# Performance work log

Measured on AMD Instinct MI355X. Metric: run time of the kernel, lower is better.

Reference implementation:

```python
import jax, jax.numpy as jnp
import numpy as np

B, S, H, D, M = 8, 1024, 16, 64, 1024


def setup_inputs() -> dict:
    key = jax.random.key(0)
    ks = jax.random.split(key, 7)
    return {
        "query_tensor": jax.random.normal(ks[0], (B, S, H, D), dtype=jnp.float32),
        "key_tensor": jax.random.normal(ks[1], (B, S, H, D), dtype=jnp.float32),
        "value_tensor": jax.random.normal(ks[2], (B, H, S, D), dtype=jnp.float32),
        "qm_b": jax.random.randint(ks[3], (M,), 0, B, dtype=jnp.int32),
        "qm_s": jax.random.randint(ks[4], (M,), 0, S, dtype=jnp.int32),
        "km_b": jax.random.randint(ks[5], (M,), 0, B, dtype=jnp.int32),
        "km_s": jax.random.randint(ks[6], (M,), 0, S, dtype=jnp.int32),
    }


def reference(query_tensor, key_tensor, value_tensor, qm_b, qm_s, km_b, km_s):
    b, s, h, d = query_tensor.shape
    scale = 1.0 / jnp.sqrt(jnp.asarray(d, jnp.float32))
    # (B,H,Sq,Sk) = Q K^T / sqrt(d); q,k given as (B,S,H,D)
    corr = jnp.einsum('bqhd,bkhd->bhqk', query_tensor, key_tensor) * scale
    # masks: query_mask zeros whole rows, key_mask zeros whole columns
    row_masked = jnp.zeros((b, s), dtype=bool).at[qm_b, qm_s].set(True)
    col_masked = jnp.zeros((b, s), dtype=bool).at[km_b, km_s].set(True)
    masked = row_masked[:, None, :, None] | col_masked[:, None, None, :]
    corr = jnp.where(masked, jnp.asarray(-1e10, corr.dtype), corr)
    attn = jax.nn.softmax(corr, axis=-1)
    # value_tensor is already (B,H,S,D) per the original (no permute applied)
    return jnp.einsum('bhqk,bhkd->bhqd', attn, value_tensor)
```

## Files before the change

### kernel.cpp

```cpp
#include <hip/hip_runtime.h>
#include <stdint.h>

#define GLOBAL_AS __attribute__((address_space(1)))
#define LDS_AS __attribute__((address_space(3)))

namespace {
constexpr int Bn = 8, Sn = 1024, Hn = 16, Dn = 64, Mn = 1024;
constexpr int BQ = 128;
constexpr int TK = 64;
constexpr int NT = Sn / TK;
constexpr int LDE = 72;
constexpr int TILE_SH = 2 * 64 * LDE;
constexpr size_t BLOB_BYTES = (size_t)Bn * Hn * NT * TILE_SH * 2;
constexpr size_t ROWM_OFF = BLOB_BYTES;
constexpr float kSC = 0.125f * 1.4426950408889634f;

using f32x16 = __attribute__((ext_vector_type(16))) float;
using s16x4 = __attribute__((ext_vector_type(4))) short;
using s16x8 = __attribute__((ext_vector_type(8))) short;

__device__ inline unsigned pk2(float a, float b) {
    union { __bf16 h[2]; unsigned u; } x;
    x.h[0] = (__bf16)a; x.h[1] = (__bf16)b;
    return x.u;
}

#if __has_builtin(__builtin_amdgcn_exp2f)
#define EXP2F __builtin_amdgcn_exp2f
#else
#define EXP2F exp2f
#endif
}

__global__ __launch_bounds__(256) void convert3(
    const float* __restrict__ K, const float* __restrict__ V,
    unsigned short* __restrict__ blob,
    const int* __restrict__ qmb, const int* __restrict__ qms,
    const int* __restrict__ kmb, const int* __restrict__ kms,
    unsigned int* __restrict__ wsm)
{
    __shared__ float Vl[64 * 65];
    const int t = threadIdx.x;
    const int kt = blockIdx.x, h = blockIdx.y, b = blockIdx.z;

    if (kt == 0 && h == 0 && b == 0) {
        #pragma unroll
        for (int i = 0; i < 9; ++i) wsm[t + 256 * i] = 0;
        __syncthreads();
        unsigned char* rowm = (unsigned char*)wsm;
        unsigned long long* colbits = (unsigned long long*)(wsm + 2048);
        #pragma unroll
        for (int i = 0; i < 4; ++i) {
            const int idx = t + 256 * i;
            rowm[qmb[idx] * Sn + qms[idx]] = 1;
            atomicOr(&colbits[kmb[idx] * NT + (kms[idx] >> 6)], 1ull << (kms[idx] & 63));
        }
    }

    unsigned short* out = blob + ((size_t)((b * Hn + h) * NT + kt)) * TILE_SH;
    const int key = t >> 2, dg = (t & 3) * 16;
    {
        const float* kp = K + (((size_t)b * Sn + kt * TK + key) * Hn + h) * Dn + dg;
        uint2 w[4];
        #pragma unroll
        for (int j = 0; j < 4; ++j) {
            float4 v = *(const float4*)(kp + j * 4);
            w[j].x = pk2(v.x, v.y); w[j].y = pk2(v.z, v.w);
        }
        uint2* o = (uint2*)&out[key * LDE + dg];
        #pragma unroll
        for (int j = 0; j < 4; ++j) o[j] = w[j];
    }
    {
        const float* vp = V + (((size_t)b * Hn + h) * Sn + kt * TK + key) * Dn + dg;
        #pragma unroll
        for (int j = 0; j < 4; ++j) {
            float4 v = *(const float4*)(vp + j * 4);
            Vl[(dg + j * 4 + 0) * 65 + key] = v.x;
            Vl[(dg + j * 4 + 1) * 65 + key] = v.y;
            Vl[(dg + j * 4 + 2) * 65 + key] = v.z;
            Vl[(dg + j * 4 + 3) * 65 + key] = v.w;
        }
    }
    __syncthreads();
    {
        const int d = t >> 2, kc = (t & 3) * 16;
        float tmp[16];
        #pragma unroll
        for (int i = 0; i < 16; ++i) tmp[i] = Vl[d * 65 + kc + i];
        uint2* o = (uint2*)&out[64 * LDE + d * LDE + kc];
        #pragma unroll
        for (int j = 0; j < 4; ++j) {
            uint2 w; w.x = pk2(tmp[j * 4 + 0], tmp[j * 4 + 1]);
            w.y = pk2(tmp[j * 4 + 2], tmp[j * 4 + 3]);
            o[j] = w;
        }
    }
}

__global__ __launch_bounds__(256, 4) void attn4(
    const float* __restrict__ Q, const unsigned short* __restrict__ blob,
    const unsigned char* __restrict__ rowm,
    const unsigned long long* __restrict__ colbits,
    float* __restrict__ Out)
{
    __shared__ unsigned short KV[TILE_SH];
    const int t = threadIdx.x;
    const int wave = t >> 6, lane = t & 63;
    const int l31 = lane & 31, q2 = lane >> 5;
    const int bh = blockIdx.x, b = bh >> 4, h = bh & 15;
    const int qb = blockIdx.y * BQ + wave * 32;

    s16x8 qf[4];
    {
        const float* qp = Q + (((size_t)b * Sn + qb + l31) * Hn + h) * Dn + q2 * 8;
        #pragma unroll
        for (int st = 0; st < 4; ++st) {
            float4 a = *(const float4*)(qp + st * 16);
            float4 c = *(const float4*)(qp + st * 16 + 4);
            union { unsigned w[4]; s16x8 v; } f;
            f.w[0] = pk2(a.x * kSC, a.y * kSC);
            f.w[1] = pk2(a.z * kSC, a.w * kSC);
            f.w[2] = pk2(c.x * kSC, c.y * kSC);
            f.w[3] = pk2(c.z * kSC, c.w * kSC);
            qf[st] = f.v;
        }
    }
    const bool rmb = rowm[b * Sn + qb + l31] != 0;
    const float rmONE = rmb ? 1.0f : 0.0f;
    const unsigned rmKEEP = rmb ? 0u : 0xFFFFFFFFu;

    f32x16 O[2];
    #pragma unroll
    for (int dt = 0; dt < 2; ++dt)
        #pragma unroll
        for (int i = 0; i < 16; ++i) O[dt][i] = 0.0f;
    float lsum = 0.0f;

    const unsigned short* tile0 = blob + (size_t)bh * NT * TILE_SH;

    for (int kt = 0; kt < NT; ++kt) {
        __syncthreads();
        {
            const GLOBAL_AS unsigned int* g =
                (const GLOBAL_AS unsigned int*)(tile0 + (size_t)kt * TILE_SH);
            LDS_AS unsigned int* l = (LDS_AS unsigned int*)KV;
            #pragma unroll
            for (int j = 0; j < 4; ++j)
                __builtin_amdgcn_global_load_lds(g + j * 1024 + t * 4,
                                                 l + j * 1024 + t * 4, 16, 0, 0);
            if (t < 128)
                __builtin_amdgcn_global_load_lds(g + 4096 + t * 4,
                                                 l + 4096 + t * 4, 16, 0, 0);
        }
        const unsigned long long cmask = colbits[b * NT + kt];
        __syncthreads();

        #pragma unroll
        for (int ct = 0; ct < 2; ++ct) {
            s16x8 kf[4];
            #pragma unroll
            for (int st = 0; st < 4; ++st)
                kf[st] = *(const s16x8*)&KV[(ct * 32 + l31) * LDE + st * 16 + q2 * 8];
            const unsigned ncm = ~(((unsigned)(cmask >> (ct * 32))) >> (q2 * 4));

            f32x16 sc;
            #pragma unroll
            for (int i = 0; i < 16; ++i) sc[i] = 0.0f;
            #pragma unroll
            for (int st = 0; st < 4; ++st)
                sc = __builtin_amdgcn_mfma_f32_32x32x16_bf16(kf[st], qf[st], sc, 0, 0, 0);

            const unsigned keep = ncm & rmKEEP;
            unsigned u[8];
            #pragma unroll
            for (int c = 0; c < 4; ++c) {
                float p[4];
                #pragma unroll
                for (int j = 0; j < 4; ++j) {
                    float e = EXP2F(sc[4 * c + j]);
                    unsigned m = (unsigned)__builtin_amdgcn_sbfe((int)keep, 8 * c + j, 1);
                    p[j] = __uint_as_float(__float_as_uint(e) & m) + rmONE;
                }
                lsum += (p[0] + p[1]) + (p[2] + p[3]);
                u[2 * c]     = pk2(p[0], p[1]);
                u[2 * c + 1] = pk2(p[2], p[3]);
            }
            s16x8 P[2];
            union { unsigned w[4]; s16x8 v; } f0, f1;
            f0.w[0] = u[0]; f0.w[1] = u[1]; f0.w[2] = u[2]; f0.w[3] = u[3];
            f1.w[0] = u[4]; f1.w[1] = u[5]; f1.w[2] = u[6]; f1.w[3] = u[7];
            P[0] = f0.v;
            P[1] = f1.v;

            const unsigned short* Vt = &KV[64 * LDE];
            #pragma unroll
            for (int dt = 0; dt < 2; ++dt)
                #pragma unroll
                for (int ch = 0; ch < 2; ++ch) {
                    const int base = (dt * 32 + l31) * LDE + ct * 32 + ch * 16 + q2 * 4;
                    s16x4 lo = *(const s16x4*)&Vt[base];
                    s16x4 hi = *(const s16x4*)&Vt[base + 8];
                    s16x8 vf = __builtin_shufflevector(lo, hi, 0, 1, 2, 3, 4, 5, 6, 7);
                    O[dt] = __builtin_amdgcn_mfma_f32_32x32x16_bf16(P[ch], vf, O[dt], 0, 0, 0);
                }
        }
    }

    const float invs = 1.0f / (lsum + __shfl_xor(lsum, 32, 64));
    float* op = Out + ((size_t)(b * Hn + h)) * Sn * Dn;
    #pragma unroll
    for (int reg = 0; reg < 16; ++reg) {
        const int qrow = (reg & 3) + 8 * (reg >> 2) + 4 * q2;
        const float invl = __shfl(invs, qrow, 64);
        const int q = qb + qrow;
        #pragma unroll
        for (int dt = 0; dt < 2; ++dt)
            op[(size_t)q * Dn + dt * 32 + l31] = O[dt][reg] * invl;
    }
}

extern "C" void kernel_launch(void* const* d_in, const int* in_sizes, int n_in,
                              void* d_out, int out_size, void* d_ws, size_t ws_size,
                              hipStream_t stream) {
    (void)in_sizes; (void)n_in; (void)out_size; (void)ws_size;
    const float* Q = (const float*)d_in[0];
    const float* K = (const float*)d_in[1];
    const float* V = (const float*)d_in[2];
    const int* qmb = (const int*)d_in[3];
    const int* qms = (const int*)d_in[4];
    const int* kmb = (const int*)d_in[5];
    const int* kms = (const int*)d_in[6];
    float* Out = (float*)d_out;

    unsigned short* blob = (unsigned short*)d_ws;
    unsigned int* wsm = (unsigned int*)(void*)((char*)d_ws + ROWM_OFF);
    const unsigned char* rowm = (const unsigned char*)wsm;
    const unsigned long long* colbits = (const unsigned long long*)(wsm + 2048);

    convert3<<<dim3(NT, Hn, Bn), 256, 0, stream>>>(K, V, blob, qmb, qms, kmb, kms, wsm);
    attn4<<<dim3(Bn * Hn, Sn / BQ), 256, 0, stream>>>(Q, blob, rowm, colbits, Out);
}
```

Measured before the change: 194.3 us.

## Fold key/query masks into an extra MFMA step via a bias column

Column-mask bits are written as a -1e8 bf16 bias into the padding columns of each K tile, and the query row mask is applied by zeroing the Q scale and adding a fifth Q fragment (1 or 0). Together these let a fifth MFMA step apply both masks inside the score computation, so the per-element bit-extract masking in the softmax loop goes away. The V transpose is permuted so each lane can fetch its fragment with one 16-byte LDS load instead of two 8-byte loads. Mask construction moves to a separate single-block kernel ahead of the convert kernel, which adds a launch and a serial dependency in exchange for 25% more QK MFMA work.

Result: faster. 186.1 us (-4.2%).

```diff
diff --git a/kernel.cpp b/kernel.cpp
--- a/kernel.cpp
+++ b/kernel.cpp
@@ -14,9 +14,9 @@
 constexpr size_t BLOB_BYTES = (size_t)Bn * Hn * NT * TILE_SH * 2;
 constexpr size_t ROWM_OFF = BLOB_BYTES;
 constexpr float kSC = 0.125f * 1.4426950408889634f;
+constexpr float kBIAS = -1e8f;
 
 using f32x16 = __attribute__((ext_vector_type(16))) float;
-using s16x4 = __attribute__((ext_vector_type(4))) short;
 using s16x8 = __attribute__((ext_vector_type(8))) short;
 
 __device__ inline unsigned pk2(float a, float b) {
@@ -32,32 +32,32 @@
 #endif
 }
 
-__global__ __launch_bounds__(256) void convert3(
-    const float* __restrict__ K, const float* __restrict__ V,
-    unsigned short* __restrict__ blob,
+__global__ __launch_bounds__(1024) void masks_k(
     const int* __restrict__ qmb, const int* __restrict__ qms,
     const int* __restrict__ kmb, const int* __restrict__ kms,
     unsigned int* __restrict__ wsm)
 {
+    const int t = threadIdx.x;
+    wsm[t] = 0; wsm[t + 1024] = 0;
+    if (t < 256) wsm[t + 2048] = 0;
+    __syncthreads();
+    unsigned char* rowm = (unsigned char*)wsm;
+    unsigned long long* colbits = (unsigned long long*)(wsm + 2048);
+    rowm[qmb[t] * Sn + qms[t]] = 1;
+    atomicOr(&colbits[kmb[t] * NT + (kms[t] >> 6)], 1ull << (kms[t] & 63));
+}
+
+__global__ __launch_bounds__(256) void convert4(
+    const float* __restrict__ K, const float* __restrict__ V,
+    unsigned short* __restrict__ blob,
+    const unsigned long long* __restrict__ colbits)
+{
     __shared__ float Vl[64 * 65];
     const int t = threadIdx.x;
     const int kt = blockIdx.x, h = blockIdx.y, b = blockIdx.z;
-
-    if (kt == 0 && h == 0 && b == 0) {
-        #pragma unroll
-        for (int i = 0; i < 9; ++i) wsm[t + 256 * i] = 0;
-        __syncthreads();
-        unsigned char* rowm = (unsigned char*)wsm;
-        unsigned long long* colbits = (unsigned long long*)(wsm + 2048);
-        #pragma unroll
-        for (int i = 0; i < 4; ++i) {
-            const int idx = t + 256 * i;
-            rowm[qmb[idx] * Sn + qms[idx]] = 1;
-            atomicOr(&colbits[kmb[idx] * NT + (kms[idx] >> 6)], 1ull << (kms[idx] & 63));
-        }
-    }
-
     unsigned short* out = blob + ((size_t)((b * Hn + h) * NT + kt)) * TILE_SH;
+    const unsigned long long cb = colbits[b * NT + kt];
+
     const int key = t >> 2, dg = (t & 3) * 16;
     {
         const float* kp = K + (((size_t)b * Sn + kt * TK + key) * Hn + h) * Dn + dg;
@@ -70,6 +70,12 @@
         uint2* o = (uint2*)&out[key * LDE + dg];
         #pragma unroll
         for (int j = 0; j < 4; ++j) o[j] = w[j];
+    }
+    if ((t & 3) == 3) {
+        const float bias = ((cb >> key) & 1ull) ? kBIAS : 0.0f;
+        uint2 w; w.x = pk2(bias, 0.0f); w.y = 0u;
+        *(uint2*)&out[key * LDE + 64] = w;
+        *(uint2*)&out[key * LDE + 68] = (uint2){0u, 0u};
     }
     {
         const float* vp = V + (((size_t)b * Hn + h) * Sn + kt * TK + key) * Dn + dg;
@@ -88,20 +94,21 @@
         float tmp[16];
         #pragma unroll
         for (int i = 0; i < 16; ++i) tmp[i] = Vl[d * 65 + kc + i];
+        const int perm[16] = {0, 1, 2, 3, 8, 9, 10, 11, 4, 5, 6, 7, 12, 13, 14, 15};
         uint2* o = (uint2*)&out[64 * LDE + d * LDE + kc];
         #pragma unroll
         for (int j = 0; j < 4; ++j) {
-            uint2 w; w.x = pk2(tmp[j * 4 + 0], tmp[j * 4 + 1]);
-            w.y = pk2(tmp[j * 4 + 2], tmp[j * 4 + 3]);
+            uint2 w;
+            w.x = pk2(tmp[perm[4 * j + 0]], tmp[perm[4 * j + 1]]);
+            w.y = pk2(tmp[perm[4 * j + 2]], tmp[perm[4 * j + 3]]);
             o[j] = w;
         }
     }
 }
 
-__global__ __launch_bounds__(256, 4) void attn4(
+__global__ __launch_bounds__(256, 4) void attn5(
     const float* __restrict__ Q, const unsigned short* __restrict__ blob,
     const unsigned char* __restrict__ rowm,
-    const unsigned long long* __restrict__ colbits,
     float* __restrict__ Out)
 {
     __shared__ unsigned short KV[TILE_SH];
@@ -111,7 +118,10 @@
     const int bh = blockIdx.x, b = bh >> 4, h = bh & 15;
     const int qb = blockIdx.y * BQ + wave * 32;
 
-    s16x8 qf[4];
+    const bool rmb = rowm[b * Sn + qb + l31] != 0;
+    const float qscale = rmb ? 0.0f : kSC;
+
+    s16x8 qf[5];
     {
         const float* qp = Q + (((size_t)b * Sn + qb + l31) * Hn + h) * Dn + q2 * 8;
         #pragma unroll
@@ -119,16 +129,17 @@
             float4 a = *(const float4*)(qp + st * 16);
             float4 c = *(const float4*)(qp + st * 16 + 4);
             union { unsigned w[4]; s16x8 v; } f;
-            f.w[0] = pk2(a.x * kSC, a.y * kSC);
-            f.w[1] = pk2(a.z * kSC, a.w * kSC);
-            f.w[2] = pk2(c.x * kSC, c.y * kSC);
-            f.w[3] = pk2(c.z * kSC, c.w * kSC);
+            f.w[0] = pk2(a.x * qscale, a.y * qscale);
+            f.w[1] = pk2(a.z * qscale, a.w * qscale);
+            f.w[2] = pk2(c.x * qscale, c.y * qscale);
+            f.w[3] = pk2(c.z * qscale, c.w * qscale);
             qf[st] = f.v;
         }
-    }
-    const bool rmb = rowm[b * Sn + qb + l31] != 0;
-    const float rmONE = rmb ? 1.0f : 0.0f;
-    const unsigned rmKEEP = rmb ? 0u : 0xFFFFFFFFu;
+        union { unsigned w[4]; s16x8 v; } f5;
+        f5.w[0] = (q2 == 0) ? pk2(rmb ? 0.0f : 1.0f, 0.0f) : 0u;
+        f5.w[1] = 0u; f5.w[2] = 0u; f5.w[3] = 0u;
+        qf[4] = f5.v;
+    }
 
     f32x16 O[2];
     #pragma unroll
@@ -153,38 +164,32 @@
                 __builtin_amdgcn_global_load_lds(g + 4096 + t * 4,
                                                  l + 4096 + t * 4, 16, 0, 0);
         }
-        const unsigned long long cmask = colbits[b * NT + kt];
         __syncthreads();
 
         #pragma unroll
         for (int ct = 0; ct < 2; ++ct) {
-            s16x8 kf[4];
-            #pragma unroll
-            for (int st = 0; st < 4; ++st)
+            s16x8 kf[5];
+            #pragma unroll
+            for (int st = 0; st < 5; ++st)
                 kf[st] = *(const s16x8*)&KV[(ct * 32 + l31) * LDE + st * 16 + q2 * 8];
-            const unsigned ncm = ~(((unsigned)(cmask >> (ct * 32))) >> (q2 * 4));
 
             f32x16 sc;
             #pragma unroll
             for (int i = 0; i < 16; ++i) sc[i] = 0.0f;
             #pragma unroll
-            for (int st = 0; st < 4; ++st)
+            for (int st = 0; st < 5; ++st)
                 sc = __builtin_amdgcn_mfma_f32_32x32x16_bf16(kf[st], qf[st], sc, 0, 0, 0);
 
-            const unsigned keep = ncm & rmKEEP;
             unsigned u[8];
             #pragma unroll
             for (int c = 0; c < 4; ++c) {
-                float p[4];
-                #pragma unroll
-                for (int j = 0; j < 4; ++j) {
-                    float e = EXP2F(sc[4 * c + j]);
-                    unsigned m = (unsigned)__builtin_amdgcn_sbfe((int)keep, 8 * c + j, 1);
-                    p[j] = __uint_as_float(__float_as_uint(e) & m) + rmONE;
-                }
-                lsum += (p[0] + p[1]) + (p[2] + p[3]);
-                u[2 * c]     = pk2(p[0], p[1]);
-                u[2 * c + 1] = pk2(p[2], p[3]);
+                float p0 = EXP2F(sc[4 * c + 0]);
+                float p1 = EXP2F(sc[4 * c + 1]);
+                float p2 = EXP2F(sc[4 * c + 2]);
+                float p3 = EXP2F(sc[4 * c + 3]);
+                lsum += (p0 + p1) + (p2 + p3);
+                u[2 * c]     = pk2(p0, p1);
+                u[2 * c + 1] = pk2(p2, p3);
             }
             s16x8 P[2];
             union { unsigned w[4]; s16x8 v; } f0, f1;
@@ -198,10 +203,7 @@
             for (int dt = 0; dt < 2; ++dt)
                 #pragma unroll
                 for (int ch = 0; ch < 2; ++ch) {
-                    const int base = (dt * 32 + l31) * LDE + ct * 32 + ch * 16 + q2 * 4;
-                    s16x4 lo = *(const s16x4*)&Vt[base];
-                    s16x4 hi = *(const s16x4*)&Vt[base + 8];
-                    s16x8 vf = __builtin_shufflevector(lo, hi, 0, 1, 2, 3, 4, 5, 6, 7);
+                    s16x8 vf = *(const s16x8*)&Vt[(dt * 32 + l31) * LDE + ct * 32 + ch * 16 + q2 * 8];
                     O[dt] = __builtin_amdgcn_mfma_f32_32x32x16_bf16(P[ch], vf, O[dt], 0, 0, 0);
                 }
         }
@@ -238,6 +240,7 @@
     const unsigned char* rowm = (const unsigned char*)wsm;
     const unsigned long long* colbits = (const unsigned long long*)(wsm + 2048);
 
-    convert3<<<dim3(NT, Hn, Bn), 256, 0, stream>>>(K, V, blob, qmb, qms, kmb, kms, wsm);
-    attn4<<<dim3(Bn * Hn, Sn / BQ), 256, 0, stream>>>(Q, blob, rowm, colbits, Out);
-}
+    masks_k<<<1, 1024, 0, stream>>>(qmb, qms, kmb, kms, wsm);
+    convert4<<<dim3(NT, Hn, Bn), 256, 0, stream>>>(K, V, blob, colbits);
+    attn5<<<dim3(Bn * Hn, Sn / BQ), 256, 0, stream>>>(Q, blob, rowm, Out);
+}
```
